# Kernel tuning notes

Measured on AMD Instinct MI355X. Metric: run time of the kernel, lower is better.

Reference implementation:

```python
import jax, jax.numpy as jnp
import numpy as np

LAYERS = 30
LAYERS_PER_STACK = 10  # layers // stacks
UPSAMPLE_SCALES = (10, 8)


def _c1x1(w, x):
    # 1x1 conv: w [O,C], x [B,C,T] -> [B,O,T]
    return jnp.einsum('oc,bct->bot', w, x)


def setup_inputs() -> dict:
    key = jax.random.key(0)
    ks = jax.random.split(key, 16)
    B, T, F = 4, 32000, 400
    s = 0.1  # weight scale to keep gates unsaturated
    inp = {
        'x': jax.random.normal(ks[0], (B, 256, T), jnp.float32),
        'c': jax.random.normal(ks[1], (B, 80, F), jnp.float32),
        'first_w': jax.random.normal(ks[2], (64, 256), jnp.float32) * s,
        'first_b': jnp.zeros((64,), jnp.float32),
        'conv_w': jax.random.normal(ks[3], (LAYERS, 128, 64, 2), jnp.float32) * s,
        'conv_b': jnp.zeros((LAYERS, 128), jnp.float32),
        'cond_w': jax.random.normal(ks[4], (LAYERS, 128, 80), jnp.float32) * s,
        'out_w': jax.random.normal(ks[5], (LAYERS, 64, 64), jnp.float32) * s,
        'out_b': jnp.zeros((LAYERS, 64), jnp.float32),
        'skip_w': jax.random.normal(ks[6], (LAYERS, 64, 64), jnp.float32) * s,
        'skip_b': jnp.zeros((LAYERS, 64), jnp.float32),
        'last1_w': jax.random.normal(ks[7], (64, 64), jnp.float32) * s,
        'last1_b': jnp.zeros((64,), jnp.float32),
        'last2_w': jax.random.normal(ks[8], (256, 64), jnp.float32) * s,
        'last2_b': jnp.zeros((256,), jnp.float32),
        'conv_in_w': jax.random.normal(ks[9], (80, 80), jnp.float32) * s,
        # upsample smoothing kernels, torch init: constant 1/kernel_size
        'up_w0': jnp.full((2 * 10 + 1,), 1.0 / (2 * 10 + 1), jnp.float32),
        'up_w1': jnp.full((2 * 8 + 1,), 1.0 / (2 * 8 + 1), jnp.float32),
    }
    return inp


def _wavenet(x, c, first_w, first_b, conv_w, conv_b, cond_w, out_w, out_b,
             skip_w, skip_b, last1_w, last1_b, last2_w, last2_b, conv_in_w,
             up_w0, up_w1):
    # --- ConvInUpsampleNetwork (aux_context_window=0 -> conv_in is 1x1, no bias) ---
    c = _c1x1(conv_in_w, c)  # [B,80,F]
    C = c.shape[1]
    for scale, w in zip(UPSAMPLE_SCALES, (up_w0, up_w1)):
        c = jnp.repeat(c, scale, axis=2)  # nearest interpolate along time
        rhs = jnp.broadcast_to(w[None, None, :], (C, 1, w.shape[0]))  # depthwise avg
        c = jax.lax.conv_general_dilated(
            c, rhs, window_strides=(1,), padding=[(scale, scale)],
            feature_group_count=C, dimension_numbers=('NCH', 'OIH', 'NCH'))
    # c now [B,80,T] with T = F*80 matching x
    T = x.shape[2]

    # --- first 1x1 conv ---
    h = _c1x1(first_w, x) + first_b[None, :, None]  # [B,64,T]

    skips = jnp.zeros_like(h[:, :64, :]) * 0.0  # [B,64,T]
    skips = 0.0
    for l in range(LAYERS):
        d = 2 ** (l % LAYERS_PER_STACK)  # dilation; padding = (k-1)*d = d
        xp = jnp.pad(h, ((0, 0), (0, 0), (d, 0)))  # causal left pad
        # dilated conv, kernel_size=2: taps at t-d and t
        g = (jnp.einsum('oc,bct->bot', conv_w[l, :, :, 0], xp[:, :, :T])
             + jnp.einsum('oc,bct->bot', conv_w[l, :, :, 1], xp[:, :, d:d + T])
             + conv_b[l][None, :, None])  # [B,128,T]
        g = g + _c1x1(cond_w[l], c)  # conditioning (split(a,b)+split(ca,cb) == split(g+cc))
        a, b = jnp.split(g, 2, axis=1)
        z = jnp.tanh(a) * jax.nn.sigmoid(b)  # [B,64,T]
        skips = skips + _c1x1(skip_w[l], z) + skip_b[l][None, :, None]
        h = h + _c1x1(out_w[l], z) + out_b[l][None, :, None]

    # --- last conv layers: ReLU, 1x1, ReLU, 1x1 ---
    o = jax.nn.relu(skips)
    o = _c1x1(last1_w, o) + last1_b[None, :, None]
    o = jax.nn.relu(o)
    o = _c1x1(last2_w, o) + last2_b[None, :, None]
    return o  # [B,256,T]


def reference(x, c, first_w, first_b, conv_w, conv_b, cond_w, out_w, out_b,
              skip_w, skip_b, last1_w, last1_b, last2_w, last2_b, conv_in_w,
              up_w0, up_w1):
    return _wavenet(x, c, first_w, first_b, conv_w, conv_b, cond_w, out_w,
                    out_b, skip_w, skip_b, last1_w, last1_b, last2_w, last2_b,
                    conv_in_w, up_w0, up_w1)
```

## Files before the change

kernel.cpp:

```cpp
#include <hip/hip_runtime.h>
#include <math.h>

#define T_TOTAL 32000
#define BATCH 4
#define TT 64

typedef __bf16 bf16x8 __attribute__((ext_vector_type(8)));
typedef float f32x4 __attribute__((ext_vector_type(4)));
typedef unsigned int uint4v __attribute__((ext_vector_type(4)));
typedef unsigned int uint2v __attribute__((ext_vector_type(2)));

__device__ __forceinline__ unsigned short f2b(float f) {
    unsigned int u = __float_as_uint(f);
    u += 0x7FFFu + ((u >> 16) & 1u);
    return (unsigned short)(u >> 16);
}
__device__ __forceinline__ unsigned int f2b2(float lo, float hi) {
    return (unsigned int)f2b(lo) | ((unsigned int)f2b(hi) << 16);
}
__device__ __forceinline__ bf16x8 ld_bf8(const unsigned short* p) {
    return __builtin_bit_cast(bf16x8, *(const uint4v*)p);
}
__device__ __forceinline__ float fast_sigmoid(float x) {
    return __builtin_amdgcn_rcpf(1.0f + __expf(-x));
}
__device__ __forceinline__ float fast_tanh(float x) {
    return 1.0f - 2.0f * __builtin_amdgcn_rcpf(1.0f + __expf(2.0f * x));
}

__global__ void k_pack(const float* __restrict__ conv_w, const float* __restrict__ cond_w,
                       const float* __restrict__ skip_w, const float* __restrict__ out_w,
                       const float* __restrict__ first_w, const float* __restrict__ last1_w,
                       const float* __restrict__ last2_w, const float* __restrict__ skip_b,
                       unsigned short* __restrict__ wgp, unsigned short* __restrict__ wzp,
                       unsigned short* __restrict__ fwp, unsigned short* __restrict__ l1p,
                       unsigned short* __restrict__ l2p, float* __restrict__ sbs, int do_sbs) {
    int i = blockIdx.x * blockDim.x + threadIdx.x;
    if (i < 860160) {
        int l = i / 28672, r = i % 28672;
        int o = r / 224, k = r % 224;
        float v;
        if (k < 64)       v = conv_w[(((size_t)l * 128 + o) * 64 + k) * 2 + 0];
        else if (k < 128) v = conv_w[(((size_t)l * 128 + o) * 64 + (k - 64)) * 2 + 1];
        else if (k < 208) v = cond_w[((size_t)l * 128 + o) * 80 + (k - 128)];
        else              v = 0.0f;
        wgp[i] = f2b(v);
        return;
    }
    i -= 860160;
    if (i < 245760) {
        int l = i / 8192, rr = (i % 8192) / 64, k = i % 64;
        float v = (rr < 64) ? skip_w[((size_t)l * 64 + rr) * 64 + k]
                            : out_w[((size_t)l * 64 + (rr - 64)) * 64 + k];
        wzp[i] = f2b(v);
        return;
    }
    i -= 245760;
    if (i < 16384) { fwp[i] = f2b(first_w[i]); return; }
    i -= 16384;
    if (i < 4096) { l1p[i] = f2b(last1_w[i]); return; }
    i -= 4096;
    if (i < 16384) { l2p[i] = f2b(last2_w[i]); return; }
    i -= 16384;
    if (i < 64 && do_sbs) {
        float a = 0.f;
        for (int l = 0; l < 30; ++l) a += skip_b[l * 64 + i];
        sbs[i] = a;
    }
}

__global__ void k_convin(const float* __restrict__ c, const float* __restrict__ w,
                         float* __restrict__ c1) {
    int idx = blockIdx.x * blockDim.x + threadIdx.x;
    if (idx >= BATCH * 80 * 400) return;
    int f = idx % 400;
    int o = (idx / 400) % 80;
    int b = idx / (400 * 80);
    const float* cb = c + (size_t)b * 80 * 400 + f;
    const float* wr = w + o * 80;
    float acc = 0.f;
    #pragma unroll 8
    for (int j = 0; j < 80; ++j) acc += wr[j] * cb[(size_t)j * 400];
    c1[idx] = acc;
}

__global__ void k_up0(const float* __restrict__ c1, const float* __restrict__ w,
                      float* __restrict__ c2) {
    int idx = blockIdx.x * blockDim.x + threadIdx.x;
    if (idx >= BATCH * 80 * 4000) return;
    int t = idx % 4000;
    int ch = idx / 4000;
    int u = t / 10, r = t - u * 10;
    float w0 = 0.f, w1 = 0.f, w2 = 0.f;
    #pragma unroll
    for (int j = 0; j < 21; ++j) {
        float wj = w[j];
        int a = r - 10 + j;
        if (a < 0) w0 += wj;
        else if (a < 10) w1 += wj;
        else w2 += wj;
    }
    const float* src = c1 + (size_t)ch * 400;
    float s0 = (u >= 1) ? src[u - 1] : 0.f;
    float s1 = src[u];
    float s2 = (u + 1 < 400) ? src[u + 1] : 0.f;
    c2[idx] = w0 * s0 + w1 * s1 + w2 * s2;
}

__global__ __launch_bounds__(256) void k_up1b(const float* __restrict__ c2,
                                              const float* __restrict__ w,
                                              unsigned short* __restrict__ cupb) {
    __shared__ float S[80][13];
    __shared__ float W[8][4];
    const int b = blockIdx.y, t0 = blockIdx.x * 64;
    const int tid = threadIdx.x;
    const int u0 = t0 >> 3;

    for (int i = tid; i < 800; i += 256) {
        int ch = i / 10, uu = i % 10;
        int u = u0 - 1 + uu;
        float v = 0.f;
        if (u >= 0 && u < 4000) v = c2[((size_t)b * 80 + ch) * 4000 + u];
        S[ch][uu] = v;
    }
    if (tid < 24) {
        int r = tid / 3, k = tid % 3;
        int jlo = (k == 0) ? 0 : (k == 1 ? 8 - r : 16 - r);
        int jhi = (k == 0) ? 7 - r : (k == 1 ? 15 - r : 16);
        float a = 0.f;
        for (int j = jlo; j <= jhi; ++j) a += w[j];
        W[r][k] = a;
    }
    __syncthreads();

    unsigned short* ob = cupb + ((size_t)b * T_TOTAL + t0) * 96;
    for (int i = tid; i < 64 * 96; i += 256) {
        int ch = i % 96;
        int tl = i / 96;
        float acc = 0.f;
        if (ch < 80) {
            int r = tl & 7, ub = tl >> 3;
            acc = W[r][0] * S[ch][ub] + W[r][1] * S[ch][ub + 1] + W[r][2] * S[ch][ub + 2];
        }
        ob[i] = f2b(acc);
    }
}

#define XFS 266
__global__ __launch_bounds__(256, 4) void k_first(
    const float* __restrict__ x, const unsigned short* __restrict__ fwp,
    const float* __restrict__ fb, float* __restrict__ h0) {
    __shared__ unsigned short Xf[64 * XFS];
    const int b = blockIdx.y, t0 = blockIdx.x * TT, tid = threadIdx.x;
    const int lane = tid & 63;
    const int wv = __builtin_amdgcn_readfirstlane(tid >> 6);
    const int l15 = lane & 15, q = lane >> 4;

    for (int i = tid; i < 4096; i += 256) {
        int ch = i >> 4;
        int t4 = (i & 15) << 2;
        const float* xr = x + ((size_t)b * 256 + ch) * T_TOTAL + t0 + t4;
        float4 u = *(const float4*)xr;
        int base = t4 * XFS + ch;
        Xf[base + 0 * XFS] = f2b(u.x);
        Xf[base + 1 * XFS] = f2b(u.y);
        Xf[base + 2 * XFS] = f2b(u.z);
        Xf[base + 3 * XFS] = f2b(u.w);
    }
    __syncthreads();

    f32x4 acc[4] = {};
    const unsigned short* wr = fwp + (size_t)(16 * wv + l15) * 256;
    #pragma unroll
    for (int ks = 0; ks < 8; ++ks) {
        bf16x8 aA = ld_bf8(wr + ks * 32 + q * 8);
        #pragma unroll
        for (int tt = 0; tt < 4; ++tt) {
            bf16x8 bb = ld_bf8(&Xf[(tt * 16 + l15) * XFS + ks * 32 + q * 8]);
            acc[tt] = __builtin_amdgcn_mfma_f32_16x16x32_bf16(aA, bb, acc[tt], 0, 0, 0);
        }
    }
    const float4 fbv = *(const float4*)&fb[16 * wv + 4 * q];
    float* hob = h0 + (size_t)b * T_TOTAL * 64;
    #pragma unroll
    for (int tt = 0; tt < 4; ++tt) {
        size_t base = (size_t)(t0 + tt * 16 + l15) * 64 + 16 * wv + 4 * q;
        float4 ho;
        ho.x = acc[tt][0] + fbv.x;
        ho.y = acc[tt][1] + fbv.y;
        ho.z = acc[tt][2] + fbv.z;
        ho.w = acc[tt][3] + fbv.w;
        *(float4*)(hob + base) = ho;
    }
}

__global__ __launch_bounds__(256, 4) void k_layer(
    const float* __restrict__ h_in, float* __restrict__ h_out,
    unsigned short* __restrict__ zb_l, const unsigned short* __restrict__ cupb,
    const unsigned short* __restrict__ wgp_l, const unsigned short* __restrict__ wzp_l,
    const float* __restrict__ cb_l, const float* __restrict__ ob_l, int d) {
    __shared__ unsigned short Xl[64 * 224];
    __shared__ unsigned short zs[64 * 72];
    const int b = blockIdx.y, t0 = blockIdx.x * TT, tid = threadIdx.x;
    const int lane = tid & 63;
    const int wv = __builtin_amdgcn_readfirstlane(tid >> 6);
    const int l15 = lane & 15, q = lane >> 4;

    const float* hb = h_in + (size_t)b * T_TOTAL * 64;
    for (int i = tid; i < 512; i += 256) {
        int t = i >> 3, cb8 = (i & 7) << 3;
        const float4* p1 = (const float4*)(hb + (size_t)(t0 + t) * 64 + cb8);
        float4 u0 = p1[0], u1 = p1[1];
        uint4v v1;
        v1.x = f2b2(u0.x, u0.y); v1.y = f2b2(u0.z, u0.w);
        v1.z = f2b2(u1.x, u1.y); v1.w = f2b2(u1.z, u1.w);
        *(uint4v*)&Xl[t * 224 + 64 + cb8] = v1;
        int td = t0 + t - d;
        uint4v v0 = {0u, 0u, 0u, 0u};
        if (td >= 0) {
            const float4* p0 = (const float4*)(hb + (size_t)td * 64 + cb8);
            float4 w0 = p0[0], w1 = p0[1];
            v0.x = f2b2(w0.x, w0.y); v0.y = f2b2(w0.z, w0.w);
            v0.z = f2b2(w1.x, w1.y); v0.w = f2b2(w1.z, w1.w);
        }
        *(uint4v*)&Xl[t * 224 + cb8] = v0;
    }
    const unsigned short* cbb = cupb + (size_t)b * T_TOTAL * 96;
    for (int i = tid; i < 768; i += 256) {
        int t = i / 12, j = (i % 12) << 3;
        *(uint4v*)&Xl[t * 224 + 128 + j] = *(const uint4v*)&cbb[(size_t)(t0 + t) * 96 + j];
    }
    __syncthreads();

    f32x4 accA[4] = {}, accG[4] = {};
    const unsigned short* wrow_a = wgp_l + (size_t)(16 * wv + l15) * 224;
    const unsigned short* wrow_g = wgp_l + (size_t)(64 + 16 * wv + l15) * 224;
    #pragma unroll
    for (int ks = 0; ks < 7; ++ks) {
        bf16x8 aA = ld_bf8(wrow_a + ks * 32 + q * 8);
        bf16x8 aG = ld_bf8(wrow_g + ks * 32 + q * 8);
        #pragma unroll
        for (int tt = 0; tt < 4; ++tt) {
            bf16x8 bb = ld_bf8(&Xl[(tt * 16 + l15) * 224 + ks * 32 + q * 8]);
            accA[tt] = __builtin_amdgcn_mfma_f32_16x16x32_bf16(aA, bb, accA[tt], 0, 0, 0);
            accG[tt] = __builtin_amdgcn_mfma_f32_16x16x32_bf16(aG, bb, accG[tt], 0, 0, 0);
        }
    }
    const float4 cbA = *(const float4*)&cb_l[16 * wv + 4 * q];
    const float4 cbG = *(const float4*)&cb_l[64 + 16 * wv + 4 * q];
    #pragma unroll
    for (int tt = 0; tt < 4; ++tt) {
        int t = tt * 16 + l15;
        float z0 = fast_tanh(accA[tt][0] + cbA.x) * fast_sigmoid(accG[tt][0] + cbG.x);
        float z1 = fast_tanh(accA[tt][1] + cbA.y) * fast_sigmoid(accG[tt][1] + cbG.y);
        float z2 = fast_tanh(accA[tt][2] + cbA.z) * fast_sigmoid(accG[tt][2] + cbG.z);
        float z3 = fast_tanh(accA[tt][3] + cbA.w) * fast_sigmoid(accG[tt][3] + cbG.w);
        uint2v zv;
        zv.x = f2b2(z0, z1);
        zv.y = f2b2(z2, z3);
        *(uint2v*)&zs[t * 72 + 16 * wv + 4 * q] = zv;
    }
    __syncthreads();

    unsigned short* zg = zb_l + ((size_t)b * T_TOTAL + t0) * 64;
    #pragma unroll
    for (int it = 0; it < 2; ++it) {
        int i = tid + it * 256;
        int t = i >> 3, c8 = (i & 7) << 3;
        *(uint4v*)&zg[t * 64 + c8] = *(const uint4v*)&zs[t * 72 + c8];
    }

    f32x4 accO[4] = {};
    const unsigned short* zrow_o = wzp_l + (size_t)(64 + 16 * wv + l15) * 64;
    #pragma unroll
    for (int ks = 0; ks < 2; ++ks) {
        bf16x8 aO = ld_bf8(zrow_o + ks * 32 + q * 8);
        #pragma unroll
        for (int tt = 0; tt < 4; ++tt) {
            bf16x8 bb = ld_bf8(&zs[(tt * 16 + l15) * 72 + ks * 32 + q * 8]);
            accO[tt] = __builtin_amdgcn_mfma_f32_16x16x32_bf16(aO, bb, accO[tt], 0, 0, 0);
        }
    }
    const float4 obv = *(const float4*)&ob_l[16 * wv + 4 * q];
    float* hob = h_out + (size_t)b * T_TOTAL * 64;
    #pragma unroll
    for (int tt = 0; tt < 4; ++tt) {
        size_t base = (size_t)(t0 + tt * 16 + l15) * 64 + 16 * wv + 4 * q;
        float4 hi = *(const float4*)(hb + base);
        float4 ho;
        ho.x = hi.x + accO[tt][0] + obv.x;
        ho.y = hi.y + accO[tt][1] + obv.y;
        ho.z = hi.z + accO[tt][2] + obv.z;
        ho.w = hi.w + accO[tt][3] + obv.w;
        *(float4*)(hob + base) = ho;
    }
}

__global__ __launch_bounds__(256, 4) void k_layer_f(
    const float* __restrict__ h_in, float* __restrict__ h_out,
    float* __restrict__ skips, const unsigned short* __restrict__ cupb,
    const unsigned short* __restrict__ wgp, const unsigned short* __restrict__ wzp,
    const float* __restrict__ cb_l, const float* __restrict__ ob_l,
    const float* __restrict__ sb_l, int d, int first) {
    __shared__ unsigned short Xl[64 * 224];
    __shared__ unsigned short zs[64 * 72];
    const int b = blockIdx.y, t0 = blockIdx.x * TT, tid = threadIdx.x;
    const int lane = tid & 63;
    const int wv = __builtin_amdgcn_readfirstlane(tid >> 6);
    const int l15 = lane & 15, q = lane >> 4;

    const float* hb = h_in + (size_t)b * T_TOTAL * 64;
    for (int i = tid; i < 512; i += 256) {
        int t = i >> 3, cb8 = (i & 7) << 3;
        const float4* p1 = (const float4*)(hb + (size_t)(t0 + t) * 64 + cb8);
        float4 u0 = p1[0], u1 = p1[1];
        uint4v v1;
        v1.x = f2b2(u0.x, u0.y); v1.y = f2b2(u0.z, u0.w);
        v1.z = f2b2(u1.x, u1.y); v1.w = f2b2(u1.z, u1.w);
        *(uint4v*)&Xl[t * 224 + 64 + cb8] = v1;
        int td = t0 + t - d;
        uint4v v0 = {0u, 0u, 0u, 0u};
        if (td >= 0) {
            const float4* p0 = (const float4*)(hb + (size_t)td * 64 + cb8);
            float4 w0 = p0[0], w1 = p0[1];
            v0.x = f2b2(w0.x, w0.y); v0.y = f2b2(w0.z, w0.w);
            v0.z = f2b2(w1.x, w1.y); v0.w = f2b2(w1.z, w1.w);
        }
        *(uint4v*)&Xl[t * 224 + cb8] = v0;
    }
    const unsigned short* cbb = cupb + (size_t)b * T_TOTAL * 96;
    for (int i = tid; i < 768; i += 256) {
        int t = i / 12, j = (i % 12) << 3;
        *(uint4v*)&Xl[t * 224 + 128 + j] = *(const uint4v*)&cbb[(size_t)(t0 + t) * 96 + j];
    }
    __syncthreads();

    f32x4 accA[4] = {}, accG[4] = {};
    const unsigned short* wrow_a = wgp + (size_t)(16 * wv + l15) * 224;
    const unsigned short* wrow_g = wgp + (size_t)(64 + 16 * wv + l15) * 224;
    #pragma unroll
    for (int ks = 0; ks < 7; ++ks) {
        bf16x8 aA = ld_bf8(wrow_a + ks * 32 + q * 8);
        bf16x8 aG = ld_bf8(wrow_g + ks * 32 + q * 8);
        #pragma unroll
        for (int tt = 0; tt < 4; ++tt) {
            bf16x8 bb = ld_bf8(&Xl[(tt * 16 + l15) * 224 + ks * 32 + q * 8]);
            accA[tt] = __builtin_amdgcn_mfma_f32_16x16x32_bf16(aA, bb, accA[tt], 0, 0, 0);
            accG[tt] = __builtin_amdgcn_mfma_f32_16x16x32_bf16(aG, bb, accG[tt], 0, 0, 0);
        }
    }
    const float4 cbA = *(const float4*)&cb_l[16 * wv + 4 * q];
    const float4 cbG = *(const float4*)&cb_l[64 + 16 * wv + 4 * q];
    #pragma unroll
    for (int tt = 0; tt < 4; ++tt) {
        int t = tt * 16 + l15;
        float z0 = fast_tanh(accA[tt][0] + cbA.x) * fast_sigmoid(accG[tt][0] + cbG.x);
        float z1 = fast_tanh(accA[tt][1] + cbA.y) * fast_sigmoid(accG[tt][1] + cbG.y);
        float z2 = fast_tanh(accA[tt][2] + cbA.z) * fast_sigmoid(accG[tt][2] + cbG.z);
        float z3 = fast_tanh(accA[tt][3] + cbA.w) * fast_sigmoid(accG[tt][3] + cbG.w);
        uint2v zv;
        zv.x = f2b2(z0, z1);
        zv.y = f2b2(z2, z3);
        *(uint2v*)&zs[t * 72 + 16 * wv + 4 * q] = zv;
    }
    __syncthreads();

    f32x4 accS[4] = {}, accO[4] = {};
    const unsigned short* zrow_s = wzp + (size_t)(16 * wv + l15) * 64;
    const unsigned short* zrow_o = wzp + (size_t)(64 + 16 * wv + l15) * 64;
    #pragma unroll
    for (int ks = 0; ks < 2; ++ks) {
        bf16x8 aS = ld_bf8(zrow_s + ks * 32 + q * 8);
        bf16x8 aO = ld_bf8(zrow_o + ks * 32 + q * 8);
        #pragma unroll
        for (int tt = 0; tt < 4; ++tt) {
            bf16x8 bb = ld_bf8(&zs[(tt * 16 + l15) * 72 + ks * 32 + q * 8]);
            accS[tt] = __builtin_amdgcn_mfma_f32_16x16x32_bf16(aS, bb, accS[tt], 0, 0, 0);
            accO[tt] = __builtin_amdgcn_mfma_f32_16x16x32_bf16(aO, bb, accO[tt], 0, 0, 0);
        }
    }
    const float4 sbv = *(const float4*)&sb_l[16 * wv + 4 * q];
    const float4 obv = *(const float4*)&ob_l[16 * wv + 4 * q];
    float* hob = h_out + (size_t)b * T_TOTAL * 64;
    float* skb = skips + (size_t)b * T_TOTAL * 64;
    #pragma unroll
    for (int tt = 0; tt < 4; ++tt) {
        size_t base = (size_t)(t0 + tt * 16 + l15) * 64 + 16 * wv + 4 * q;
        float4 hi = *(const float4*)(hb + base);
        float4 ho;
        ho.x = hi.x + accO[tt][0] + obv.x;
        ho.y = hi.y + accO[tt][1] + obv.y;
        ho.z = hi.z + accO[tt][2] + obv.z;
        ho.w = hi.w + accO[tt][3] + obv.w;
        *(float4*)(hob + base) = ho;
        float4 sv;
        if (first) {
            sv.x = accS[tt][0] + sbv.x;
            sv.y = accS[tt][1] + sbv.y;
            sv.z = accS[tt][2] + sbv.z;
            sv.w = accS[tt][3] + sbv.w;
        } else {
            float4 sp = *(const float4*)(skb + base);
            sv.x = sp.x + accS[tt][0] + sbv.x;
            sv.y = sp.y + accS[tt][1] + sbv.y;
            sv.z = sp.z + accS[tt][2] + sbv.z;
            sv.w = sp.w + accS[tt][3] + sbv.w;
        }
        *(float4*)(skb + base) = sv;
    }
}

__global__ __launch_bounds__(256) void k_skips(
    const unsigned short* __restrict__ zbuf, const unsigned short* __restrict__ wzp,
    const float* __restrict__ sbs, const unsigned short* __restrict__ l1p,
    const float* __restrict__ b1, const unsigned short* __restrict__ l2p,
    const float* __restrict__ b2, float* __restrict__ out) {
    __shared__ unsigned short zt[64 * 72];
    __shared__ unsigned short o2s[64 * 72];
    const int b = blockIdx.y, t0 = blockIdx.x * TT, tid = threadIdx.x;
    const int lane = tid & 63;
    const int wv = __builtin_amdgcn_readfirstlane(tid >> 6);
    const int l15 = lane & 15, q = lane >> 4;

    const int st_t = tid >> 3, st_c = (tid & 7) << 3;
    const int st_t2 = (tid + 256) >> 3, st_c2 = ((tid + 256) & 7) << 3;
    const unsigned short* zb = zbuf + ((size_t)b * T_TOTAL + t0) * 64;

    f32x4 acc[4] = {};
    for (int l = 0; l < 30; ++l) {
        const unsigned short* src = zb + (size_t)l * BATCH * T_TOTAL * 64;
        *(uint4v*)&zt[st_t * 72 + st_c] = *(const uint4v*)&src[st_t * 64 + st_c];
        *(uint4v*)&zt[st_t2 * 72 + st_c2] = *(const uint4v*)&src[st_t2 * 64 + st_c2];
        __syncthreads();
        const unsigned short* wr = wzp + (size_t)l * 8192 + (size_t)(16 * wv + l15) * 64;
        #pragma unroll
        for (int ks = 0; ks < 2; ++ks) {
            bf16x8 aS = ld_bf8(wr + ks * 32 + q * 8);
            #pragma unroll
            for (int tt = 0; tt < 4; ++tt) {
                bf16x8 bb = ld_bf8(&zt[(tt * 16 + l15) * 72 + ks * 32 + q * 8]);
                acc[tt] = __builtin_amdgcn_mfma_f32_16x16x32_bf16(aS, bb, acc[tt], 0, 0, 0);
            }
        }
        __syncthreads();
    }

    const float4 sbv = *(const float4*)&sbs[16 * wv + 4 * q];
    #pragma unroll
    for (int tt = 0; tt < 4; ++tt) {
        int t = tt * 16 + l15;
        float s0 = fmaxf(acc[tt][0] + sbv.x, 0.f);
        float s1 = fmaxf(acc[tt][1] + sbv.y, 0.f);
        float s2 = fmaxf(acc[tt][2] + sbv.z, 0.f);
        float s3 = fmaxf(acc[tt][3] + sbv.w, 0.f);
        uint2v zv;
        zv.x = f2b2(s0, s1);
        zv.y = f2b2(s2, s3);
        *(uint2v*)&zt[t * 72 + 16 * wv + 4 * q] = zv;
    }
    __syncthreads();

    f32x4 a1[4] = {};
    const unsigned short* w1r = l1p + (size_t)(16 * wv + l15) * 64;
    #pragma unroll
    for (int ks = 0; ks < 2; ++ks) {
        bf16x8 aA = ld_bf8(w1r + ks * 32 + q * 8);
        #pragma unroll
        for (int tt = 0; tt < 4; ++tt) {
            bf16x8 bb = ld_bf8(&zt[(tt * 16 + l15) * 72 + ks * 32 + q * 8]);
            a1[tt] = __builtin_amdgcn_mfma_f32_16x16x32_bf16(aA, bb, a1[tt], 0, 0, 0);
        }
    }
    const float4 b1v = *(const float4*)&b1[16 * wv + 4 * q];
    #pragma unroll
    for (int tt = 0; tt < 4; ++tt) {
        int t = tt * 16 + l15;
        float z0 = fmaxf(a1[tt][0] + b1v.x, 0.f);
        float z1 = fmaxf(a1[tt][1] + b1v.y, 0.f);
        float z2 = fmaxf(a1[tt][2] + b1v.z, 0.f);
        float z3 = fmaxf(a1[tt][3] + b1v.w, 0.f);
        uint2v zv;
        zv.x = f2b2(z0, z1);
        zv.y = f2b2(z2, z3);
        *(uint2v*)&o2s[t * 72 + 16 * wv + 4 * q] = zv;
    }
    __syncthreads();

    f32x4 a2[4][4] = {};
    #pragma unroll
    for (int ks = 0; ks < 2; ++ks) {
        bf16x8 aw[4];
        #pragma unroll
        for (int j = 0; j < 4; ++j)
            aw[j] = ld_bf8(l2p + (size_t)(64 * wv + 16 * j + l15) * 64 + ks * 32 + q * 8);
        #pragma unroll
        for (int tt = 0; tt < 4; ++tt) {
            bf16x8 bb = ld_bf8(&o2s[(tt * 16 + l15) * 72 + ks * 32 + q * 8]);
            #pragma unroll
            for (int j = 0; j < 4; ++j)
                a2[j][tt] = __builtin_amdgcn_mfma_f32_16x16x32_bf16(aw[j], bb, a2[j][tt], 0, 0, 0);
        }
    }
    float* ob = out + (size_t)b * 256 * T_TOTAL;
    #pragma unroll
    for (int j = 0; j < 4; ++j) {
        int o0 = 64 * wv + 16 * j + 4 * q;
        float4 b2v = *(const float4*)&b2[o0];
        #pragma unroll
        for (int tt = 0; tt < 4; ++tt) {
            int t = t0 + tt * 16 + l15;
            ob[(size_t)(o0 + 0) * T_TOTAL + t] = a2[j][tt][0] + b2v.x;
            ob[(size_t)(o0 + 1) * T_TOTAL + t] = a2[j][tt][1] + b2v.y;
            ob[(size_t)(o0 + 2) * T_TOTAL + t] = a2[j][tt][2] + b2v.z;
            ob[(size_t)(o0 + 3) * T_TOTAL + t] = a2[j][tt][3] + b2v.w;
        }
    }
}

__global__ __launch_bounds__(256) void k_last(
    const float* __restrict__ skips, const unsigned short* __restrict__ l1p,
    const float* __restrict__ b1, const unsigned short* __restrict__ l2p,
    const float* __restrict__ b2, float* __restrict__ out) {
    __shared__ unsigned short sp[64 * 72];
    __shared__ unsigned short o2s[64 * 72];
    const int b = blockIdx.y, t0 = blockIdx.x * TT, tid = threadIdx.x;
    const int lane = tid & 63;
    const int wv = __builtin_amdgcn_readfirstlane(tid >> 6);
    const int l15 = lane & 15, q = lane >> 4;

    const float* skb = skips + (size_t)b * T_TOTAL * 64;
    for (int i = tid; i < 512; i += 256) {
        int t = i >> 3, cb8 = (i & 7) << 3;
        const float4* p = (const float4*)(skb + (size_t)(t0 + t) * 64 + cb8);
        float4 u0 = p[0], u1 = p[1];
        uint4v v;
        v.x = f2b2(fmaxf(u0.x, 0.f), fmaxf(u0.y, 0.f));
        v.y = f2b2(fmaxf(u0.z, 0.f), fmaxf(u0.w, 0.f));
        v.z = f2b2(fmaxf(u1.x, 0.f), fmaxf(u1.y, 0.f));
        v.w = f2b2(fmaxf(u1.z, 0.f), fmaxf(u1.w, 0.f));
        *(uint4v*)&sp[t * 72 + cb8] = v;
    }
    __syncthreads();

    f32x4 a1[4] = {};
    const unsigned short* w1r = l1p + (size_t)(16 * wv + l15) * 64;
    #pragma unroll
    for (int ks = 0; ks < 2; ++ks) {
        bf16x8 aA = ld_bf8(w1r + ks * 32 + q * 8);
        #pragma unroll
        for (int tt = 0; tt < 4; ++tt) {
            bf16x8 bb = ld_bf8(&sp[(tt * 16 + l15) * 72 + ks * 32 + q * 8]);
            a1[tt] = __builtin_amdgcn_mfma_f32_16x16x32_bf16(aA, bb, a1[tt], 0, 0, 0);
        }
    }
    const float4 b1v = *(const float4*)&b1[16 * wv + 4 * q];
    #pragma unroll
    for (int tt = 0; tt < 4; ++tt) {
        int t = tt * 16 + l15;
        float z0 = fmaxf(a1[tt][0] + b1v.x, 0.f);
        float z1 = fmaxf(a1[tt][1] + b1v.y, 0.f);
        float z2 = fmaxf(a1[tt][2] + b1v.z, 0.f);
        float z3 = fmaxf(a1[tt][3] + b1v.w, 0.f);
        uint2v zv;
        zv.x = f2b2(z0, z1);
        zv.y = f2b2(z2, z3);
        *(uint2v*)&o2s[t * 72 + 16 * wv + 4 * q] = zv;
    }
    __syncthreads();

    f32x4 a2[4][4] = {};
    #pragma unroll
    for (int ks = 0; ks < 2; ++ks) {
        bf16x8 aw[4];
        #pragma unroll
        for (int j = 0; j < 4; ++j)
            aw[j] = ld_bf8(l2p + (size_t)(64 * wv + 16 * j + l15) * 64 + ks * 32 + q * 8);
        #pragma unroll
        for (int tt = 0; tt < 4; ++tt) {
            bf16x8 bb = ld_bf8(&o2s[(tt * 16 + l15) * 72 + ks * 32 + q * 8]);
            #pragma unroll
            for (int j = 0; j < 4; ++j)
                a2[j][tt] = __builtin_amdgcn_mfma_f32_16x16x32_bf16(aw[j], bb, a2[j][tt], 0, 0, 0);
        }
    }
    float* ob = out + (size_t)b * 256 * T_TOTAL;
    #pragma unroll
    for (int j = 0; j < 4; ++j) {
        int o0 = 64 * wv + 16 * j + 4 * q;
        float4 b2v = *(const float4*)&b2[o0];
        #pragma unroll
        for (int tt = 0; tt < 4; ++tt) {
            int t = t0 + tt * 16 + l15;
            ob[(size_t)(o0 + 0) * T_TOTAL + t] = a2[j][tt][0] + b2v.x;
            ob[(size_t)(o0 + 1) * T_TOTAL + t] = a2[j][tt][1] + b2v.y;
            ob[(size_t)(o0 + 2) * T_TOTAL + t] = a2[j][tt][2] + b2v.z;
            ob[(size_t)(o0 + 3) * T_TOTAL + t] = a2[j][tt][3] + b2v.w;
        }
    }
}

extern "C" void kernel_launch(void* const* d_in, const int* in_sizes, int n_in,
                              void* d_out, int out_size, void* d_ws, size_t ws_size,
                              hipStream_t stream) {
    const float* x         = (const float*)d_in[0];
    const float* c         = (const float*)d_in[1];
    const float* first_w   = (const float*)d_in[2];
    const float* first_b   = (const float*)d_in[3];
    const float* conv_w    = (const float*)d_in[4];
    const float* conv_b    = (const float*)d_in[5];
    const float* cond_w    = (const float*)d_in[6];
    const float* out_w     = (const float*)d_in[7];
    const float* out_b     = (const float*)d_in[8];
    const float* skip_w    = (const float*)d_in[9];
    const float* skip_b    = (const float*)d_in[10];
    const float* last1_w   = (const float*)d_in[11];
    const float* last1_b   = (const float*)d_in[12];
    const float* last2_w   = (const float*)d_in[13];
    const float* last2_b   = (const float*)d_in[14];
    const float* conv_in_w = (const float*)d_in[15];
    const float* up_w0     = (const float*)d_in[16];
    const float* up_w1     = (const float*)d_in[17];

    unsigned char* base = (unsigned char*)d_ws;
    const size_t NEED_BIG = 589549824ull;
    const bool big = ws_size >= NEED_BIG;

    dim3 grid(T_TOTAL / TT, BATCH);
    dim3 upg(T_TOTAL / 64, BATCH);

    if (big) {
        float* c1            = (float*)(base + 0);
        float* c2            = (float*)(base + 512000);
        unsigned short* cupb = (unsigned short*)(base + 5632000);
        float* hA            = (float*)(base + 30208000);
        float* hB            = (float*)(base + 62976000);
        unsigned short* wgp  = (unsigned short*)(base + 95744000);
        unsigned short* wzp  = (unsigned short*)(base + 97464320);
        unsigned short* fwp  = (unsigned short*)(base + 97955840);
        unsigned short* l1p  = (unsigned short*)(base + 97988608);
        unsigned short* l2p  = (unsigned short*)(base + 97996800);
        float* sbs           = (float*)(base + 98029568);
        unsigned short* zbuf = (unsigned short*)(base + 98029824);

        k_pack<<<(1142848 + 255) / 256, 256, 0, stream>>>(
            conv_w, cond_w, skip_w, out_w, first_w, last1_w, last2_w, skip_b,
            wgp, wzp, fwp, l1p, l2p, sbs, 1);
        k_convin<<<(BATCH * 80 * 400 + 255) / 256, 256, 0, stream>>>(c, conv_in_w, c1);
        k_up0<<<(BATCH * 80 * 4000 + 255) / 256, 256, 0, stream>>>(c1, up_w0, c2);
        k_up1b<<<upg, 256, 0, stream>>>(c2, up_w1, cupb);

        k_first<<<grid, 256, 0, stream>>>(x, fwp, first_b, hA);

        float* hin = hA;
        float* hout = hB;
        for (int l = 0; l < 30; ++l) {
            int d = 1 << (l % 10);
            k_layer<<<grid, 256, 0, stream>>>(
                hin, hout, zbuf + (size_t)l * BATCH * T_TOTAL * 64, cupb,
                wgp + (size_t)l * 128 * 224, wzp + (size_t)l * 128 * 64,
                conv_b + (size_t)l * 128, out_b + (size_t)l * 64, d);
            float* tmp = hin; hin = hout; hout = tmp;
        }

        k_skips<<<grid, 256, 0, stream>>>(zbuf, wzp, sbs, l1p, last1_b, l2p, last2_b,
                                          (float*)d_out);
    } else {
        float* c1            = (float*)(base + 0);
        float* c2            = (float*)(base + 512000);
        unsigned short* cupb = (unsigned short*)(base + 5632000);
        float* hA            = (float*)(base + 30208000);
        float* hB            = (float*)(base + 62976000);
        float* skips         = (float*)(base + 95744000);
        unsigned short* wgp  = (unsigned short*)(base + 128512000);
        unsigned short* wzp  = (unsigned short*)(base + 130232320);
        unsigned short* fwp  = (unsigned short*)(base + 130723840);
        unsigned short* l1p  = (unsigned short*)(base + 130756608);
        unsigned short* l2p  = (unsigned short*)(base + 130764800);

        k_pack<<<(1142848 + 255) / 256, 256, 0, stream>>>(
            conv_w, cond_w, skip_w, out_w, first_w, last1_w, last2_w, skip_b,
            wgp, wzp, fwp, l1p, l2p, (float*)base, 0);
        k_convin<<<(BATCH * 80 * 400 + 255) / 256, 256, 0, stream>>>(c, conv_in_w, c1);
        k_up0<<<(BATCH * 80 * 4000 + 255) / 256, 256, 0, stream>>>(c1, up_w0, c2);
        k_up1b<<<upg, 256, 0, stream>>>(c2, up_w1, cupb);

        k_first<<<grid, 256, 0, stream>>>(x, fwp, first_b, hA);

        float* hin = hA;
        float* hout = hB;
        for (int l = 0; l < 30; ++l) {
            int d = 1 << (l % 10);
            k_layer_f<<<grid, 256, 0, stream>>>(
                hin, hout, skips, cupb,
                wgp + (size_t)l * 128 * 224, wzp + (size_t)l * 128 * 64,
                conv_b + (size_t)l * 128, out_b + (size_t)l * 64, skip_b + (size_t)l * 64,
                d, l == 0 ? 1 : 0);
            float* tmp = hin; hin = hout; hout = tmp;
        }

        k_last<<<grid, 256, 0, stream>>>(skips, l1p, last1_b, l2p, last2_b, (float*)d_out);
    }
}
```

Measured before the change: 1.493 ms.

## Chunk stored gate activations in two halves so the z-buffer path fits smaller workspace

The per-layer bf16 z buffer now keeps 15 slots instead of 30. A partial skip reduction runs after layer 15 into an fp32 buffer, and a second reduction folds the remaining layers plus the final ReLU/1x1 head. This lowers the workspace needed to take the deferred-skip path, so it can run in place of the fused per-layer skip-accumulate path. In exchange it adds one fp32 partial-sum write and read plus an extra launch. Separately, k_first now uses 32-timestep tiles and requests higher occupancy.

Result: no change. 1.505 ms (+0.8%).

```diff
diff --git a/kernel.cpp b/kernel.cpp
--- a/kernel.cpp
+++ b/kernel.cpp
@@ -4,6 +4,9 @@
 #define T_TOTAL 32000
 #define BATCH 4
 #define TT 64
+#define TTF 32
+#define ZCHUNK 15
+#define ZSLOT_ELEMS ((size_t)BATCH * T_TOTAL * 64)
 
 typedef __bf16 bf16x8 __attribute__((ext_vector_type(8)));
 typedef float f32x4 __attribute__((ext_vector_type(4)));
@@ -34,7 +37,7 @@
                        const float* __restrict__ last2_w, const float* __restrict__ skip_b,
                        unsigned short* __restrict__ wgp, unsigned short* __restrict__ wzp,
                        unsigned short* __restrict__ fwp, unsigned short* __restrict__ l1p,
-                       unsigned short* __restrict__ l2p, float* __restrict__ sbs, int do_sbs) {
+                       unsigned short* __restrict__ l2p, float* __restrict__ sbs) {
     int i = blockIdx.x * blockDim.x + threadIdx.x;
     if (i < 860160) {
         int l = i / 28672, r = i % 28672;
@@ -62,7 +65,7 @@
     i -= 4096;
     if (i < 16384) { l2p[i] = f2b(last2_w[i]); return; }
     i -= 16384;
-    if (i < 64 && do_sbs) {
+    if (i < 64) {
         float a = 0.f;
         for (int l = 0; l < 30; ++l) a += skip_b[l * 64 + i];
         sbs[i] = a;
@@ -147,18 +150,18 @@
 }
 
 #define XFS 266
-__global__ __launch_bounds__(256, 4) void k_first(
+__global__ __launch_bounds__(256, 8) void k_first(
     const float* __restrict__ x, const unsigned short* __restrict__ fwp,
     const float* __restrict__ fb, float* __restrict__ h0) {
-    __shared__ unsigned short Xf[64 * XFS];
-    const int b = blockIdx.y, t0 = blockIdx.x * TT, tid = threadIdx.x;
+    __shared__ unsigned short Xf[TTF * XFS];
+    const int b = blockIdx.y, t0 = blockIdx.x * TTF, tid = threadIdx.x;
     const int lane = tid & 63;
     const int wv = __builtin_amdgcn_readfirstlane(tid >> 6);
     const int l15 = lane & 15, q = lane >> 4;
 
-    for (int i = tid; i < 4096; i += 256) {
-        int ch = i >> 4;
-        int t4 = (i & 15) << 2;
+    for (int i = tid; i < 2048; i += 256) {
+        int ch = i >> 3;
+        int t4 = (i & 7) << 2;
         const float* xr = x + ((size_t)b * 256 + ch) * T_TOTAL + t0 + t4;
         float4 u = *(const float4*)xr;
         int base = t4 * XFS + ch;
@@ -169,13 +172,13 @@
     }
     __syncthreads();
 
-    f32x4 acc[4] = {};
+    f32x4 acc[2] = {};
     const unsigned short* wr = fwp + (size_t)(16 * wv + l15) * 256;
     #pragma unroll
     for (int ks = 0; ks < 8; ++ks) {
         bf16x8 aA = ld_bf8(wr + ks * 32 + q * 8);
         #pragma unroll
-        for (int tt = 0; tt < 4; ++tt) {
+        for (int tt = 0; tt < 2; ++tt) {
             bf16x8 bb = ld_bf8(&Xf[(tt * 16 + l15) * XFS + ks * 32 + q * 8]);
             acc[tt] = __builtin_amdgcn_mfma_f32_16x16x32_bf16(aA, bb, acc[tt], 0, 0, 0);
         }
@@ -183,7 +186,7 @@
     const float4 fbv = *(const float4*)&fb[16 * wv + 4 * q];
     float* hob = h0 + (size_t)b * T_TOTAL * 64;
     #pragma unroll
-    for (int tt = 0; tt < 4; ++tt) {
+    for (int tt = 0; tt < 2; ++tt) {
         size_t base = (size_t)(t0 + tt * 16 + l15) * 64 + 16 * wv + 4 * q;
         float4 ho;
         ho.x = acc[tt][0] + fbv.x;
@@ -411,7 +414,8 @@
 }
 
 __global__ __launch_bounds__(256) void k_skips(
-    const unsigned short* __restrict__ zbuf, const unsigned short* __restrict__ wzp,
+    const unsigned short* __restrict__ zbuf, const unsigned short* __restrict__ wzp_c,
+    int nl, float* __restrict__ partial, int mode,
     const float* __restrict__ sbs, const unsigned short* __restrict__ l1p,
     const float* __restrict__ b1, const unsigned short* __restrict__ l2p,
     const float* __restrict__ b2, float* __restrict__ out) {
@@ -427,12 +431,12 @@
     const unsigned short* zb = zbuf + ((size_t)b * T_TOTAL + t0) * 64;
 
     f32x4 acc[4] = {};
-    for (int l = 0; l < 30; ++l) {
-        const unsigned short* src = zb + (size_t)l * BATCH * T_TOTAL * 64;
+    for (int l = 0; l < nl; ++l) {
+        const unsigned short* src = zb + (size_t)l * ZSLOT_ELEMS;
         *(uint4v*)&zt[st_t * 72 + st_c] = *(const uint4v*)&src[st_t * 64 + st_c];
         *(uint4v*)&zt[st_t2 * 72 + st_c2] = *(const uint4v*)&src[st_t2 * 64 + st_c2];
         __syncthreads();
-        const unsigned short* wr = wzp + (size_t)l * 8192 + (size_t)(16 * wv + l15) * 64;
+        const unsigned short* wr = wzp_c + (size_t)l * 8192 + (size_t)(16 * wv + l15) * 64;
         #pragma unroll
         for (int ks = 0; ks < 2; ++ks) {
             bf16x8 aS = ld_bf8(wr + ks * 32 + q * 8);
@@ -445,14 +449,28 @@
         __syncthreads();
     }
 
+    float* pb = partial + (size_t)b * T_TOTAL * 64;
+    if (mode == 0) {
+        #pragma unroll
+        for (int tt = 0; tt < 4; ++tt) {
+            size_t base = (size_t)(t0 + tt * 16 + l15) * 64 + 16 * wv + 4 * q;
+            float4 sv;
+            sv.x = acc[tt][0]; sv.y = acc[tt][1]; sv.z = acc[tt][2]; sv.w = acc[tt][3];
+            *(float4*)(pb + base) = sv;
+        }
+        return;
+    }
+
     const float4 sbv = *(const float4*)&sbs[16 * wv + 4 * q];
     #pragma unroll
     for (int tt = 0; tt < 4; ++tt) {
         int t = tt * 16 + l15;
-        float s0 = fmaxf(acc[tt][0] + sbv.x, 0.f);
-        float s1 = fmaxf(acc[tt][1] + sbv.y, 0.f);
-        float s2 = fmaxf(acc[tt][2] + sbv.z, 0.f);
-        float s3 = fmaxf(acc[tt][3] + sbv.w, 0.f);
+        size_t base = (size_t)(t0 + t) * 64 + 16 * wv + 4 * q;
+        float4 sp = *(const float4*)(pb + base);
+        float s0 = fmaxf(sp.x + acc[tt][0] + sbv.x, 0.f);
+        float s1 = fmaxf(sp.y + acc[tt][1] + sbv.y, 0.f);
+        float s2 = fmaxf(sp.z + acc[tt][2] + sbv.z, 0.f);
+        float s3 = fmaxf(sp.w + acc[tt][3] + sbv.w, 0.f);
         uint2v zv;
         zv.x = f2b2(s0, s1);
         zv.y = f2b2(s2, s3);
@@ -622,82 +640,65 @@
     const float* up_w1     = (const float*)d_in[17];
 
     unsigned char* base = (unsigned char*)d_ws;
-    const size_t NEED_BIG = 589549824ull;
-    const bool big = ws_size >= NEED_BIG;
+    float* c1            = (float*)(base + 0);
+    float* c2            = (float*)(base + 512000);
+    unsigned short* cupb = (unsigned short*)(base + 5632000);
+    float* hA            = (float*)(base + 30208000);
+    float* hB            = (float*)(base + 62976000);
+    float* skipsP        = (float*)(base + 95744000);
+    unsigned short* wgp  = (unsigned short*)(base + 128512000);
+    unsigned short* wzp  = (unsigned short*)(base + 130232320);
+    unsigned short* fwp  = (unsigned short*)(base + 130723840);
+    unsigned short* l1p  = (unsigned short*)(base + 130756608);
+    unsigned short* l2p  = (unsigned short*)(base + 130764800);
+    float* sbs           = (float*)(base + 130797568);
+    unsigned short* zbuf = (unsigned short*)(base + 130797824);
+
+    const bool big = ws_size >= 376557824ull;
+
+    k_pack<<<(1142848 + 255) / 256, 256, 0, stream>>>(
+        conv_w, cond_w, skip_w, out_w, first_w, last1_w, last2_w, skip_b,
+        wgp, wzp, fwp, l1p, l2p, sbs);
+    k_convin<<<(BATCH * 80 * 400 + 255) / 256, 256, 0, stream>>>(c, conv_in_w, c1);
+    k_up0<<<(BATCH * 80 * 4000 + 255) / 256, 256, 0, stream>>>(c1, up_w0, c2);
+    dim3 upg(T_TOTAL / 64, BATCH);
+    k_up1b<<<upg, 256, 0, stream>>>(c2, up_w1, cupb);
+
+    dim3 gridF(T_TOTAL / TTF, BATCH);
+    k_first<<<gridF, 256, 0, stream>>>(x, fwp, first_b, hA);
 
     dim3 grid(T_TOTAL / TT, BATCH);
-    dim3 upg(T_TOTAL / 64, BATCH);
+    float* hin = hA;
+    float* hout = hB;
 
     if (big) {
-        float* c1            = (float*)(base + 0);
-        float* c2            = (float*)(base + 512000);
-        unsigned short* cupb = (unsigned short*)(base + 5632000);
-        float* hA            = (float*)(base + 30208000);
-        float* hB            = (float*)(base + 62976000);
-        unsigned short* wgp  = (unsigned short*)(base + 95744000);
-        unsigned short* wzp  = (unsigned short*)(base + 97464320);
-        unsigned short* fwp  = (unsigned short*)(base + 97955840);
-        unsigned short* l1p  = (unsigned short*)(base + 97988608);
-        unsigned short* l2p  = (unsigned short*)(base + 97996800);
-        float* sbs           = (float*)(base + 98029568);
-        unsigned short* zbuf = (unsigned short*)(base + 98029824);
-
-        k_pack<<<(1142848 + 255) / 256, 256, 0, stream>>>(
-            conv_w, cond_w, skip_w, out_w, first_w, last1_w, last2_w, skip_b,
-            wgp, wzp, fwp, l1p, l2p, sbs, 1);
-        k_convin<<<(BATCH * 80 * 400 + 255) / 256, 256, 0, stream>>>(c, conv_in_w, c1);
-        k_up0<<<(BATCH * 80 * 4000 + 255) / 256, 256, 0, stream>>>(c1, up_w0, c2);
-        k_up1b<<<upg, 256, 0, stream>>>(c2, up_w1, cupb);
-
-        k_first<<<grid, 256, 0, stream>>>(x, fwp, first_b, hA);
-
-        float* hin = hA;
-        float* hout = hB;
         for (int l = 0; l < 30; ++l) {
             int d = 1 << (l % 10);
+            int sl = l % ZCHUNK;
             k_layer<<<grid, 256, 0, stream>>>(
-                hin, hout, zbuf + (size_t)l * BATCH * T_TOTAL * 64, cupb,
+                hin, hout, zbuf + (size_t)sl * ZSLOT_ELEMS, cupb,
                 wgp + (size_t)l * 128 * 224, wzp + (size_t)l * 128 * 64,
                 conv_b + (size_t)l * 128, out_b + (size_t)l * 64, d);
+            if (l == ZCHUNK - 1) {
+                k_skips<<<grid, 256, 0, stream>>>(zbuf, wzp, ZCHUNK, skipsP, 0,
+                                                  sbs, l1p, last1_b, l2p, last2_b,
+                                                  (float*)d_out);
+            }
             float* tmp = hin; hin = hout; hout = tmp;
         }
-
-        k_skips<<<grid, 256, 0, stream>>>(zbuf, wzp, sbs, l1p, last1_b, l2p, last2_b,
+        k_skips<<<grid, 256, 0, stream>>>(zbuf, wzp + (size_t)ZCHUNK * 8192, ZCHUNK,
+                                          skipsP, 1, sbs, l1p, last1_b, l2p, last2_b,
                                           (float*)d_out);
     } else {
-        float* c1            = (float*)(base + 0);
-        float* c2            = (float*)(base + 512000);
-        unsigned short* cupb = (unsigned short*)(base + 5632000);
-        float* hA            = (float*)(base + 30208000);
-        float* hB            = (float*)(base + 62976000);
-        float* skips         = (float*)(base + 95744000);
-        unsigned short* wgp  = (unsigned short*)(base + 128512000);
-        unsigned short* wzp  = (unsigned short*)(base + 130232320);
-        unsigned short* fwp  = (unsigned short*)(base + 130723840);
-        unsigned short* l1p  = (unsigned short*)(base + 130756608);
-        unsigned short* l2p  = (unsigned short*)(base + 130764800);
-
-        k_pack<<<(1142848 + 255) / 256, 256, 0, stream>>>(
-            conv_w, cond_w, skip_w, out_w, first_w, last1_w, last2_w, skip_b,
-            wgp, wzp, fwp, l1p, l2p, (float*)base, 0);
-        k_convin<<<(BATCH * 80 * 400 + 255) / 256, 256, 0, stream>>>(c, conv_in_w, c1);
-        k_up0<<<(BATCH * 80 * 4000 + 255) / 256, 256, 0, stream>>>(c1, up_w0, c2);
-        k_up1b<<<upg, 256, 0, stream>>>(c2, up_w1, cupb);
-
-        k_first<<<grid, 256, 0, stream>>>(x, fwp, first_b, hA);
-
-        float* hin = hA;
-        float* hout = hB;
         for (int l = 0; l < 30; ++l) {
             int d = 1 << (l % 10);
             k_layer_f<<<grid, 256, 0, stream>>>(
-                hin, hout, skips, cupb,
+                hin, hout, skipsP, cupb,
                 wgp + (size_t)l * 128 * 224, wzp + (size_t)l * 128 * 64,
                 conv_b + (size_t)l * 128, out_b + (size_t)l * 64, skip_b + (size_t)l * 64,
                 d, l == 0 ? 1 : 0);
             float* tmp = hin; hin = hout; hout = tmp;
         }
-
-        k_last<<<grid, 256, 0, stream>>>(skips, l1p, last1_b, l2p, last2_b, (float*)d_out);
-    }
-}
+        k_last<<<grid, 256, 0, stream>>>(skipsP, l1p, last1_b, l2p, last2_b, (float*)d_out);
+    }
+}
```
